# Performance work log

Measured on AMD Instinct MI355X. Metric: run time of the kernel, lower is better.

The kernel has to match this reference:

```python
import jax, jax.numpy as jnp
import numpy as np

IDIM = 1024
HIDDEN = 4096
N_EXPERT = 8
T = 2048


def setup_inputs() -> dict:
    key = jax.random.key(0)
    ks = jax.random.split(key, 6)
    s_in = 1.0 / np.sqrt(IDIM)
    s_h = 1.0 / np.sqrt(HIDDEN)
    return {
        "xs": jax.random.normal(ks[0], (T, IDIM), dtype=jnp.float32),
        "top_k": 2,
        # gate: Linear(idim -> n_expert, bias=False); torch weight (E, D)
        "Wg": jax.random.uniform(ks[1], (N_EXPERT, IDIM), jnp.float32, -s_in, s_in),
        # experts stacked: w_1 Linear(idim->hidden), w_2 Linear(hidden->idim)
        "W1": jax.random.uniform(ks[2], (N_EXPERT, IDIM, HIDDEN), jnp.float32, -s_in, s_in),
        "b1": jax.random.uniform(ks[3], (N_EXPERT, HIDDEN), jnp.float32, -s_in, s_in),
        "W2": jax.random.uniform(ks[4], (N_EXPERT, HIDDEN, IDIM), jnp.float32, -s_h, s_h),
        "b2": jax.random.uniform(ks[5], (N_EXPERT, IDIM), jnp.float32, -s_h, s_h),
    }


def reference(xs, top_k, Wg, W1, b1, W2, b2):
    # Router: (T, E)
    router = xs @ Wg.T
    logits, selected = jax.lax.top_k(router, top_k)          # (T, k)
    # softmax over the top-k slot axis in fp32, cast back (matches torch)
    weights = jax.nn.softmax(logits.astype(jnp.float32), axis=-1).astype(xs.dtype)
    # combine weight per token per expert: (T, E). Tokens not routed to an
    # expert get weight 0, zeroing that expert's contribution (same math as
    # the masked gather / scatter-add in the torch loop).
    onehot = jax.nn.one_hot(selected, N_EXPERT, dtype=xs.dtype)  # (T, k, E)
    comb = jnp.einsum("tk,tke->te", weights, onehot)
    # all-expert FFN (dropout_rate = 0 -> identity)
    h = jax.nn.relu(jnp.einsum("td,edh->teh", xs, W1) + b1[None, :, :])
    y = jnp.einsum("teh,ehd->ted", h, W2) + b2[None, :, :]
    return jnp.einsum("te,ted->td", comb, y)
```

## Files before the change

### kernel.cpp

```cpp
#include <hip/hip_runtime.h>
#include <hip/hip_bf16.h>
#include <stdint.h>

#define T_TOK 2048
#define IDIM  1024
#define HID   4096
#define NE    8
#define BM    128
#define BN    128
#define BK    64
#define RMAX  5120
#define MAXTILES 40

typedef __bf16 bf16;
typedef bf16  bf16x8 __attribute__((ext_vector_type(8)));
typedef float f32x4  __attribute__((ext_vector_type(4)));

#define WS_NTILES   128
#define WS_TILE_E   192
#define WS_TILE_R   448
#define WS_TOK_E    1024
#define WS_TOK_W    17408
#define WS_ROW_TOK  33792
#define WS_ROW_W    54272
#define WS_H        131072
#define WS_MIN_FAST ((size_t)WS_H + (size_t)RMAX * (HID / 32) * 2)

__global__ __launch_bounds__(256) void k_zero_out(float4* __restrict__ a) {
    a[blockIdx.x * 256 + threadIdx.x] = make_float4(0.f, 0.f, 0.f, 0.f);
}

__global__ __launch_bounds__(256) void k_router(const float* __restrict__ xs,
                                                const float* __restrict__ Wg,
                                                int* __restrict__ tok_e,
                                                float* __restrict__ tok_w) {
    __shared__ float sWg[NE * IDIM];
    for (int i = threadIdx.x; i < NE * IDIM; i += 256) sWg[i] = Wg[i];
    __syncthreads();
    int wave = threadIdx.x >> 6, lane = threadIdx.x & 63;
    int t = blockIdx.x * 4 + wave;
    if (t >= T_TOK) return;
    float p[NE];
#pragma unroll
    for (int e = 0; e < NE; e++) p[e] = 0.f;
    for (int j = 0; j < IDIM / 64; j++) {
        float x = xs[(size_t)t * IDIM + j * 64 + lane];
#pragma unroll
        for (int e = 0; e < NE; e++)
            p[e] += x * sWg[e * IDIM + j * 64 + lane];
    }
#pragma unroll
    for (int e = 0; e < NE; e++) {
        float v = p[e];
        for (int off = 32; off > 0; off >>= 1) v += __shfl_down(v, off);
        p[e] = v;
    }
    if (lane == 0) {
        int e0 = 0; float l0 = p[0];
        for (int e = 1; e < NE; e++) if (p[e] > l0) { l0 = p[e]; e0 = e; }
        int e1 = -1; float l1 = -1e30f;
        for (int e = 0; e < NE; e++) if (e != e0 && p[e] > l1) { l1 = p[e]; e1 = e; }
        if (e1 < 0) e1 = (e0 + 1) & 7;
        float z = __expf(l1 - l0);
        tok_e[2 * t]     = e0;  tok_e[2 * t + 1] = e1;
        tok_w[2 * t]     = 1.f / (1.f + z);
        tok_w[2 * t + 1] = z / (1.f + z);
    }
}

__global__ __launch_bounds__(256) void k_setup(int* __restrict__ w,
                                               float* __restrict__ wf) {
    __shared__ int cnt[NE];
    __shared__ int cur[NE];
    int tid = threadIdx.x;
    if (tid < NE) cnt[tid] = 0;
    for (int i = tid; i < RMAX; i += 256) w[WS_ROW_TOK / 4 + i] = -1;
    __syncthreads();
    for (int i = tid; i < 2 * T_TOK; i += 256)
        atomicAdd(&cnt[w[WS_TOK_E / 4 + i]], 1);
    __syncthreads();
    if (tid == 0) {
        int off = 0, nt = 0;
        for (int e = 0; e < NE; e++) {
            cur[e] = off;
            int nb = (cnt[e] + BM - 1) / BM;
            for (int b = 0; b < nb && nt < MAXTILES; b++) {
                w[WS_TILE_E / 4 + nt] = e;
                w[WS_TILE_R / 4 + nt] = off + b * BM;
                nt++;
            }
            off += nb * BM;
        }
        w[WS_NTILES / 4] = nt;
    }
    __syncthreads();
    for (int i = tid; i < 2 * T_TOK; i += 256) {
        int e   = w[WS_TOK_E / 4 + i];
        int pos = atomicAdd(&cur[e], 1);
        if (pos < RMAX) {
            w[WS_ROW_TOK / 4 + pos] = i >> 1;
            wf[WS_ROW_W / 4 + pos]  = wf[WS_TOK_W / 4 + i];
        }
    }
}

__device__ inline uint4 pack8(float4 a, float4 b) {
    union { bf16 h[8]; uint4 u; } pk;
    pk.h[0] = (bf16)a.x; pk.h[1] = (bf16)a.y; pk.h[2] = (bf16)a.z; pk.h[3] = (bf16)a.w;
    pk.h[4] = (bf16)b.x; pk.h[5] = (bf16)b.y; pk.h[6] = (bf16)b.z; pk.h[7] = (bf16)b.w;
    return pk.u;
}
__device__ inline uint32_t pack2(float a, float b) {
    union { bf16 h[2]; uint32_t u; } pk;
    pk.h[0] = (bf16)a; pk.h[1] = (bf16)b;
    return pk.u;
}

__global__ __launch_bounds__(256) void k_ffn1(const float* __restrict__ xs,
                                              const float* __restrict__ W1,
                                              const float* __restrict__ b1,
                                              const int* __restrict__ wsi,
                                              bf16* __restrict__ H,
                                              int h0, int CW) {
    int ntiles = wsi[WS_NTILES / 4];
    int tile = blockIdx.y;
    if (tile >= ntiles) return;
    int e    = wsi[WS_TILE_E / 4 + tile];
    int row0 = wsi[WS_TILE_R / 4 + tile];
    int n0l  = blockIdx.x * BN;
    int n0g  = h0 + n0l;

    const int*   row_tok = wsi + WS_ROW_TOK / 4;
    const float* Be      = W1 + (size_t)e * IDIM * HID;
    const float* bias_e  = b1 + (size_t)e * HID;

    __shared__ bf16 sA[BM * BK];
    __shared__ bf16 sB[BN * 72];

    int t    = threadIdx.x;
    int lane = t & 63, wv = t >> 6;
    int wx = wv & 1, wy = wv >> 1;
    int lm = lane & 15, q = lane >> 4;

    int rtk[4];
#pragma unroll
    for (int i = 0; i < 4; i++) rtk[i] = row_tok[row0 + (t >> 3) + i * 32];

    f32x4 acc[4][4];
#pragma unroll
    for (int i = 0; i < 4; i++)
#pragma unroll
        for (int j = 0; j < 4; j++) acc[i][j] = (f32x4){0.f, 0.f, 0.f, 0.f};

    for (int kc = 0; kc < IDIM / BK; kc++) {
        if (kc) __syncthreads();
#pragma unroll
        for (int i = 0; i < 4; i++) {
            int u = t + i * 256;
            int row = u >> 3, k8 = (u & 7) * 8;
            uint4 v;
            if (rtk[i] >= 0) {
                const float* g = xs + (size_t)rtk[i] * IDIM + kc * BK + k8;
                v = pack8(*(const float4*)g, *(const float4*)(g + 4));
            } else v = make_uint4(0u, 0u, 0u, 0u);
            *(uint4*)&sA[row * BK + k8] = v;
        }
#pragma unroll
        for (int i = 0; i < 2; i++) {
            int u = t + i * 256;
            int noct = u & 15, kp = u >> 4;
            int k = kp * 2;
            const float* g = Be + (size_t)(kc * BK + k) * HID + n0g + noct * 8;
            float4 r0a = *(const float4*)g;
            float4 r0b = *(const float4*)(g + 4);
            float4 r1a = *(const float4*)(g + HID);
            float4 r1b = *(const float4*)(g + HID + 4);
            float a0[8] = {r0a.x, r0a.y, r0a.z, r0a.w, r0b.x, r0b.y, r0b.z, r0b.w};
            float a1[8] = {r1a.x, r1a.y, r1a.z, r1a.w, r1b.x, r1b.y, r1b.z, r1b.w};
            int kswz = k ^ ((noct & 3) * 16);
            int hwb  = noct * 8 * 72 + kswz;
#pragma unroll
            for (int j = 0; j < 8; j++)
                *(uint32_t*)&sB[hwb + j * 72] = pack2(a0[j], a1[j]);
        }
        __syncthreads();
#pragma unroll
        for (int ks = 0; ks < 2; ks++) {
            bf16x8 aF[4], bF[4];
#pragma unroll
            for (int mt = 0; mt < 4; mt++)
                aF[mt] = *(bf16x8*)&sA[(wy * 64 + mt * 16 + lm) * BK + ks * 32 + q * 8];
#pragma unroll
            for (int nt = 0; nt < 4; nt++) {
                int n  = wx * 64 + nt * 16 + lm;
                int kk = (ks * 32 + q * 8) ^ (((n >> 3) & 3) * 16);
                bF[nt] = *(bf16x8*)&sB[n * 72 + kk];
            }
#pragma unroll
            for (int mt = 0; mt < 4; mt++)
#pragma unroll
                for (int nt = 0; nt < 4; nt++)
                    acc[mt][nt] = __builtin_amdgcn_mfma_f32_16x16x32_bf16(
                        aF[mt], bF[nt], acc[mt][nt], 0, 0, 0);
        }
    }

#pragma unroll
    for (int nt = 0; nt < 4; nt++) {
        int col_l = n0l + wx * 64 + nt * 16 + lm;
        float bv  = bias_e[h0 + col_l];
#pragma unroll
        for (int mt = 0; mt < 4; mt++) {
            int rloc = wy * 64 + mt * 16 + q * 4;
#pragma unroll
            for (int r = 0; r < 4; r++) {
                float v = fmaxf(acc[mt][nt][r] + bv, 0.f);
                H[(size_t)(row0 + rloc + r) * CW + col_l] = (bf16)v;
            }
        }
    }
}

__global__ __launch_bounds__(256) void k_ffn2(const bf16* __restrict__ H,
                                              const float* __restrict__ W2,
                                              const float* __restrict__ b2,
                                              const int* __restrict__ wsi,
                                              const float* __restrict__ wsf,
                                              float* __restrict__ out,
                                              int h0, int CW, int addb) {
    int ntiles = wsi[WS_NTILES / 4];
    int tile = blockIdx.y;
    if (tile >= ntiles) return;
    int e    = wsi[WS_TILE_E / 4 + tile];
    int row0 = wsi[WS_TILE_R / 4 + tile];
    int n0   = blockIdx.x * BN;
    int kw   = CW / gridDim.z;
    int kb   = blockIdx.z * kw;

    const int*   row_tok = wsi + WS_ROW_TOK / 4;
    const float* row_w   = wsf + WS_ROW_W / 4;
    const float* Be      = W2 + (size_t)e * HID * IDIM;
    const float* bias_e  = b2 + (size_t)e * IDIM;

    __shared__ bf16 sA[BM * BK];
    __shared__ bf16 sB[BN * 72];

    int t    = threadIdx.x;
    int lane = t & 63, wv = t >> 6;
    int wx = wv & 1, wy = wv >> 1;
    int lm = lane & 15, q = lane >> 4;

    f32x4 acc[4][4];
#pragma unroll
    for (int i = 0; i < 4; i++)
#pragma unroll
        for (int j = 0; j < 4; j++) acc[i][j] = (f32x4){0.f, 0.f, 0.f, 0.f};

    int kiters = kw / BK;
    for (int kc = 0; kc < kiters; kc++) {
        if (kc) __syncthreads();
#pragma unroll
        for (int i = 0; i < 4; i++) {
            int u = t + i * 256;
            int row = u >> 3, k8 = (u & 7) * 8;
            *(uint4*)&sA[row * BK + k8] =
                *(const uint4*)&H[(size_t)(row0 + row) * CW + kb + kc * BK + k8];
        }
#pragma unroll
        for (int i = 0; i < 2; i++) {
            int u = t + i * 256;
            int noct = u & 15, kp = u >> 4;
            int k = kp * 2;
            const float* g = Be + (size_t)(h0 + kb + kc * BK + k) * IDIM + n0 + noct * 8;
            float4 r0a = *(const float4*)g;
            float4 r0b = *(const float4*)(g + 4);
            float4 r1a = *(const float4*)(g + IDIM);
            float4 r1b = *(const float4*)(g + IDIM + 4);
            float a0[8] = {r0a.x, r0a.y, r0a.z, r0a.w, r0b.x, r0b.y, r0b.z, r0b.w};
            float a1[8] = {r1a.x, r1a.y, r1a.z, r1a.w, r1b.x, r1b.y, r1b.z, r1b.w};
            int kswz = k ^ ((noct & 3) * 16);
            int hwb  = noct * 8 * 72 + kswz;
#pragma unroll
            for (int j = 0; j < 8; j++)
                *(uint32_t*)&sB[hwb + j * 72] = pack2(a0[j], a1[j]);
        }
        __syncthreads();
#pragma unroll
        for (int ks = 0; ks < 2; ks++) {
            bf16x8 aF[4], bF[4];
#pragma unroll
            for (int mt = 0; mt < 4; mt++)
                aF[mt] = *(bf16x8*)&sA[(wy * 64 + mt * 16 + lm) * BK + ks * 32 + q * 8];
#pragma unroll
            for (int nt = 0; nt < 4; nt++) {
                int n  = wx * 64 + nt * 16 + lm;
                int kk = (ks * 32 + q * 8) ^ (((n >> 3) & 3) * 16);
                bF[nt] = *(bf16x8*)&sB[n * 72 + kk];
            }
#pragma unroll
            for (int mt = 0; mt < 4; mt++)
#pragma unroll
                for (int nt = 0; nt < 4; nt++)
                    acc[mt][nt] = __builtin_amdgcn_mfma_f32_16x16x32_bf16(
                        aF[mt], bF[nt], acc[mt][nt], 0, 0, 0);
        }
    }

    int   tokr[16];
    float wr[16];
#pragma unroll
    for (int mt = 0; mt < 4; mt++)
#pragma unroll
        for (int r = 0; r < 4; r++) {
            int rg = row0 + wy * 64 + mt * 16 + q * 4 + r;
            tokr[mt * 4 + r] = row_tok[rg];
            wr[mt * 4 + r]   = row_w[rg];
        }
    int dobias = addb && (blockIdx.z == 0);
#pragma unroll
    for (int nt = 0; nt < 4; nt++) {
        int col  = n0 + wx * 64 + nt * 16 + lm;
        float bv = dobias ? bias_e[col] : 0.f;
#pragma unroll
        for (int mt = 0; mt < 4; mt++)
#pragma unroll
            for (int r = 0; r < 4; r++) {
                int tok = tokr[mt * 4 + r];
                if (tok >= 0)
                    atomicAdd(&out[(size_t)tok * IDIM + col],
                              wr[mt * 4 + r] * (acc[mt][nt][r] + bv));
            }
    }
}

__global__ __launch_bounds__(256) void k_fallback(const float* __restrict__ xs,
                                                  const float* __restrict__ Wg,
                                                  const float* __restrict__ W1,
                                                  const float* __restrict__ b1,
                                                  const float* __restrict__ W2,
                                                  const float* __restrict__ b2,
                                                  float* __restrict__ out) {
    __shared__ float xbuf[IDIM];
    __shared__ float hbuf[256];
    __shared__ float slog[NE];
    __shared__ int   sel[2];
    __shared__ float selw[2];

    int t   = blockIdx.x;
    int tid = threadIdx.x;

    for (int i = tid; i < IDIM; i += 256)
        xbuf[i] = xs[(size_t)t * IDIM + i];
    __syncthreads();
    {
        int e = tid >> 5, l = tid & 31;
        float p = 0.f;
        for (int d = l; d < IDIM; d += 32)
            p += xbuf[d] * Wg[e * IDIM + d];
        for (int off = 16; off > 0; off >>= 1) p += __shfl_down(p, off, 32);
        if (l == 0) slog[e] = p;
    }
    __syncthreads();
    if (tid == 0) {
        int e0 = 0; float l0 = slog[0];
        for (int e = 1; e < NE; e++) if (slog[e] > l0) { l0 = slog[e]; e0 = e; }
        int e1 = -1; float l1 = -1e30f;
        for (int e = 0; e < NE; e++) if (e != e0 && slog[e] > l1) { l1 = slog[e]; e1 = e; }
        if (e1 < 0) e1 = (e0 + 1) & 7;
        float z = __expf(l1 - l0);
        sel[0] = e0; sel[1] = e1;
        selw[0] = 1.f / (1.f + z);
        selw[1] = z / (1.f + z);
    }
    __syncthreads();

    float ytot[4] = {0.f, 0.f, 0.f, 0.f};
#pragma unroll
    for (int s = 0; s < 2; s++) {
        int   e = sel[s];
        float w = selw[s];
        const float* W1e = W1 + (size_t)e * IDIM * HID;
        const float* W2e = W2 + (size_t)e * HID * IDIM;
        float ys[4] = {0.f, 0.f, 0.f, 0.f};
        for (int hb = 0; hb < HID / 256; hb++) {
            int h = hb * 256 + tid;
            float acc = b1[e * HID + h];
            for (int d = 0; d < IDIM; d++)
                acc += xbuf[d] * W1e[(size_t)d * HID + h];
            __syncthreads();
            hbuf[tid] = fmaxf(acc, 0.f);
            __syncthreads();
            for (int hh = 0; hh < 256; hh++) {
                float hv = hbuf[hh];
                const float* wrow = W2e + (size_t)(hb * 256 + hh) * IDIM;
#pragma unroll
                for (int cc = 0; cc < 4; cc++)
                    ys[cc] += hv * wrow[cc * 256 + tid];
            }
        }
#pragma unroll
        for (int cc = 0; cc < 4; cc++)
            ytot[cc] += w * (ys[cc] + b2[e * IDIM + cc * 256 + tid]);
    }
#pragma unroll
    for (int cc = 0; cc < 4; cc++)
        out[(size_t)t * IDIM + cc * 256 + tid] = ytot[cc];
}

extern "C" void kernel_launch(void* const* d_in, const int* in_sizes, int n_in,
                              void* d_out, int out_size, void* d_ws, size_t ws_size,
                              hipStream_t stream) {
    int o = (n_in >= 7 && in_sizes[1] == 1) ? 1 : 0;
    const float* xs = (const float*)d_in[0];
    const float* Wg = (const float*)d_in[1 + o];
    const float* W1 = (const float*)d_in[2 + o];
    const float* b1 = (const float*)d_in[3 + o];
    const float* W2 = (const float*)d_in[4 + o];
    const float* b2 = (const float*)d_in[5 + o];
    float* out = (float*)d_out;

    if (ws_size < WS_MIN_FAST || d_ws == nullptr) {
        k_fallback<<<T_TOK, 256, 0, stream>>>(xs, Wg, W1, b1, W2, b2, out);
        return;
    }

    char*  ws  = (char*)d_ws;
    int*   wsi = (int*)d_ws;
    float* wsf = (float*)d_ws;
    bf16*  H   = (bf16*)(ws + WS_H);

    int HC = 1;
    while (HC < 32 &&
           (size_t)WS_H + (size_t)RMAX * (HID / HC) * 2 > ws_size)
        HC <<= 1;
    int CW = HID / HC;
    int SK = 4;
    while (CW / SK < BK) SK >>= 1;

    k_zero_out<<<T_TOK, 256, 0, stream>>>((float4*)out);
    k_router<<<T_TOK / 4, 256, 0, stream>>>(xs, Wg, wsi + WS_TOK_E / 4,
                                            wsf + WS_TOK_W / 4);
    k_setup<<<1, 256, 0, stream>>>(wsi, wsf);

    for (int c = 0; c < HC; c++) {
        k_ffn1<<<dim3(CW / BN, MAXTILES), 256, 0, stream>>>(
            xs, W1, b1, wsi, H, c * CW, CW);
        k_ffn2<<<dim3(IDIM / BN, MAXTILES, SK), 256, 0, stream>>>(
            H, W2, b2, wsi, wsf, out, c * CW, CW, c == 0 ? 1 : 0);
    }
}
```

Measured before the change: 515.7 us.

## Pre-convert weights and gathered activations to swizzled bf16, load via global_load_lds

Adds a gather kernel that packs routed token rows into a bf16 buffer and a conversion kernel that transposes and converts W1/W2 into k-contiguous, XOR-swizzled bf16 tiles in the workspace. The FFN GEMMs then stream tiles straight into LDS with global_load_lds, with no in-loop fp32-to-bf16 conversion or scattered activation reads. FFN2 drops split-K in favour of narrower 64-column tiles, which cuts the atomic traffic to the output. The cost is extra passes that read all weights and write a bf16 copy on every call, plus a larger workspace requirement.

```diff
diff --git a/kernel.cpp b/kernel.cpp
--- a/kernel.cpp
+++ b/kernel.cpp
@@ -1,5 +1,4 @@
 #include <hip/hip_runtime.h>
-#include <hip/hip_bf16.h>
 #include <stdint.h>
 
 #define T_TOK 2048
@@ -8,6 +7,7 @@
 #define NE    8
 #define BM    128
 #define BN    128
+#define BN2   64
 #define BK    64
 #define RMAX  5120
 #define MAXTILES 40
@@ -23,8 +23,7 @@
 #define WS_TOK_W    17408
 #define WS_ROW_TOK  33792
 #define WS_ROW_W    54272
-#define WS_H        131072
-#define WS_MIN_FAST ((size_t)WS_H + (size_t)RMAX * (HID / 32) * 2)
+#define XG_OFF      131072
 
 __global__ __launch_bounds__(256) void k_zero_out(float4* __restrict__ a) {
     a[blockIdx.x * 256 + threadIdx.x] = make_float4(0.f, 0.f, 0.f, 0.f);
@@ -116,35 +115,86 @@
     return pk.u;
 }
 
-__global__ __launch_bounds__(256) void k_ffn1(const float* __restrict__ xs,
-                                              const float* __restrict__ W1,
-                                              const float* __restrict__ b1,
-                                              const int* __restrict__ wsi,
-                                              bf16* __restrict__ H,
-                                              int h0, int CW) {
-    int ntiles = wsi[WS_NTILES / 4];
+__device__ __forceinline__ void g2l16(const bf16* g, bf16* l) {
+    __builtin_amdgcn_global_load_lds(
+        (const __attribute__((address_space(1))) void*)g,
+        (__attribute__((address_space(3))) void*)l, 16, 0, 0);
+}
+
+__global__ __launch_bounds__(256) void k_gather(const float* __restrict__ xs,
+                                                const int* __restrict__ wsi,
+                                                bf16* __restrict__ Xg) {
+    int wv = threadIdx.x >> 6, lane = threadIdx.x & 63;
+    int r = blockIdx.x * 4 + wv;
+    int tok = wsi[WS_ROW_TOK / 4 + r];
+#pragma unroll
+    for (int i = 0; i < 2; i++) {
+        int c = i * 64 + lane;
+        uint4 v;
+        if (tok >= 0) {
+            const float* g = xs + (size_t)tok * IDIM + c * 8;
+            v = pack8(*(const float4*)g, *(const float4*)(g + 4));
+        } else v = make_uint4(0u, 0u, 0u, 0u);
+        int cs = (c & ~7) | ((c & 7) ^ (r & 7));
+        *(uint4*)&Xg[(size_t)r * IDIM + cs * 8] = v;
+    }
+}
+
+__global__ __launch_bounds__(256) void k_cvt(const float* __restrict__ src,
+                                             bf16* __restrict__ dst,
+                                             int ld_src, int k0, int n0, int KL,
+                                             size_t s_estride, size_t d_estride) {
+    __shared__ bf16 sT[64 * 66];
+    int e = blockIdx.y;
+    const float* S = src + (size_t)e * s_estride;
+    bf16* D = dst + (size_t)e * d_estride;
+    int ntk = KL >> 6;
+    int tk = blockIdx.x % ntk, tn = blockIdx.x / ntk;
+    int t = threadIdx.x;
+#pragma unroll
+    for (int i = 0; i < 4; i++) {
+        int idx = t + i * 256;
+        int k = idx >> 4, n4 = (idx & 15) * 4;
+        float4 v = *(const float4*)&S[(size_t)(k0 + tk * 64 + k) * ld_src +
+                                      n0 + tn * 64 + n4];
+        *(uint32_t*)&sT[k * 66 + n4]     = pack2(v.x, v.y);
+        *(uint32_t*)&sT[k * 66 + n4 + 2] = pack2(v.z, v.w);
+    }
+    __syncthreads();
+#pragma unroll
+    for (int j = 0; j < 2; j++) {
+        int idx = t + j * 256;
+        int n = idx >> 3, kq = idx & 7;
+        union { bf16 h[8]; uint4 u; } pk;
+#pragma unroll
+        for (int jj = 0; jj < 8; jj++) pk.h[jj] = sT[(kq * 8 + jj) * 66 + n];
+        int ng = tn * 64 + n;
+        int ch = kq ^ (ng & 7);
+        *(uint4*)&D[(size_t)ng * KL + tk * 64 + ch * 8] = pk.u;
+    }
+}
+
+__global__ __launch_bounds__(256) void k_ffn1n(const bf16* __restrict__ Xg,
+                                               const bf16* __restrict__ W1t,
+                                               const float* __restrict__ b1,
+                                               const int* __restrict__ wsi,
+                                               bf16* __restrict__ H,
+                                               int h0, int CW) {
     int tile = blockIdx.y;
-    if (tile >= ntiles) return;
+    if (tile >= wsi[WS_NTILES / 4]) return;
     int e    = wsi[WS_TILE_E / 4 + tile];
     int row0 = wsi[WS_TILE_R / 4 + tile];
-    int n0l  = blockIdx.x * BN;
-    int n0g  = h0 + n0l;
-
-    const int*   row_tok = wsi + WS_ROW_TOK / 4;
-    const float* Be      = W1 + (size_t)e * IDIM * HID;
-    const float* bias_e  = b1 + (size_t)e * HID;
+    int n0   = blockIdx.x * BN;
+
+    const bf16* Abase = Xg + (size_t)row0 * IDIM;
+    const bf16* Bbase = W1t + ((size_t)e * CW + n0) * IDIM;
 
     __shared__ bf16 sA[BM * BK];
-    __shared__ bf16 sB[BN * 72];
-
-    int t    = threadIdx.x;
-    int lane = t & 63, wv = t >> 6;
-    int wx = wv & 1, wy = wv >> 1;
+    __shared__ bf16 sB[BN * BK];
+
+    int t = threadIdx.x, lane = t & 63;
+    int wv = t >> 6, wx = wv & 1, wy = wv >> 1;
     int lm = lane & 15, q = lane >> 4;
-
-    int rtk[4];
-#pragma unroll
-    for (int i = 0; i < 4; i++) rtk[i] = row_tok[row0 + (t >> 3) + i * 32];
 
     f32x4 acc[4][4];
 #pragma unroll
@@ -156,45 +206,29 @@
         if (kc) __syncthreads();
 #pragma unroll
         for (int i = 0; i < 4; i++) {
-            int u = t + i * 256;
-            int row = u >> 3, k8 = (u & 7) * 8;
-            uint4 v;
-            if (rtk[i] >= 0) {
-                const float* g = xs + (size_t)rtk[i] * IDIM + kc * BK + k8;
-                v = pack8(*(const float4*)g, *(const float4*)(g + 4));
-            } else v = make_uint4(0u, 0u, 0u, 0u);
-            *(uint4*)&sA[row * BK + k8] = v;
-        }
-#pragma unroll
-        for (int i = 0; i < 2; i++) {
-            int u = t + i * 256;
-            int noct = u & 15, kp = u >> 4;
-            int k = kp * 2;
-            const float* g = Be + (size_t)(kc * BK + k) * HID + n0g + noct * 8;
-            float4 r0a = *(const float4*)g;
-            float4 r0b = *(const float4*)(g + 4);
-            float4 r1a = *(const float4*)(g + HID);
-            float4 r1b = *(const float4*)(g + HID + 4);
-            float a0[8] = {r0a.x, r0a.y, r0a.z, r0a.w, r0b.x, r0b.y, r0b.z, r0b.w};
-            float a1[8] = {r1a.x, r1a.y, r1a.z, r1a.w, r1b.x, r1b.y, r1b.z, r1b.w};
-            int kswz = k ^ ((noct & 3) * 16);
-            int hwb  = noct * 8 * 72 + kswz;
-#pragma unroll
-            for (int j = 0; j < 8; j++)
-                *(uint32_t*)&sB[hwb + j * 72] = pack2(a0[j], a1[j]);
+            int s = t + i * 256;
+            g2l16(Abase + (size_t)(s >> 3) * IDIM + kc * BK + (s & 7) * 8,
+                  &sA[s * 8]);
+        }
+#pragma unroll
+        for (int i = 0; i < 4; i++) {
+            int s = t + i * 256;
+            g2l16(Bbase + (size_t)(s >> 3) * IDIM + kc * BK + (s & 7) * 8,
+                  &sB[s * 8]);
         }
         __syncthreads();
 #pragma unroll
         for (int ks = 0; ks < 2; ks++) {
             bf16x8 aF[4], bF[4];
 #pragma unroll
-            for (int mt = 0; mt < 4; mt++)
-                aF[mt] = *(bf16x8*)&sA[(wy * 64 + mt * 16 + lm) * BK + ks * 32 + q * 8];
+            for (int mt = 0; mt < 4; mt++) {
+                int r = wy * 64 + mt * 16 + lm;
+                aF[mt] = *(const bf16x8*)&sA[r * BK + (((ks * 4 + q) ^ (r & 7)) * 8)];
+            }
 #pragma unroll
             for (int nt = 0; nt < 4; nt++) {
-                int n  = wx * 64 + nt * 16 + lm;
-                int kk = (ks * 32 + q * 8) ^ (((n >> 3) & 3) * 16);
-                bF[nt] = *(bf16x8*)&sB[n * 72 + kk];
+                int r = wx * 64 + nt * 16 + lm;
+                bF[nt] = *(const bf16x8*)&sB[r * BK + (((ks * 4 + q) ^ (r & 7)) * 8)];
             }
 #pragma unroll
             for (int mt = 0; mt < 4; mt++)
@@ -204,103 +238,86 @@
                         aF[mt], bF[nt], acc[mt][nt], 0, 0, 0);
         }
     }
-
 #pragma unroll
     for (int nt = 0; nt < 4; nt++) {
-        int col_l = n0l + wx * 64 + nt * 16 + lm;
-        float bv  = bias_e[h0 + col_l];
+        int col = n0 + wx * 64 + nt * 16 + lm;
+        float bv = b1[(size_t)e * HID + h0 + col];
 #pragma unroll
         for (int mt = 0; mt < 4; mt++) {
-            int rloc = wy * 64 + mt * 16 + q * 4;
 #pragma unroll
             for (int r = 0; r < 4; r++) {
+                int rg = row0 + wy * 64 + mt * 16 + q * 4 + r;
                 float v = fmaxf(acc[mt][nt][r] + bv, 0.f);
-                H[(size_t)(row0 + rloc + r) * CW + col_l] = (bf16)v;
-            }
-        }
-    }
-}
-
-__global__ __launch_bounds__(256) void k_ffn2(const bf16* __restrict__ H,
-                                              const float* __restrict__ W2,
-                                              const float* __restrict__ b2,
-                                              const int* __restrict__ wsi,
-                                              const float* __restrict__ wsf,
-                                              float* __restrict__ out,
-                                              int h0, int CW, int addb) {
-    int ntiles = wsi[WS_NTILES / 4];
+                int sc = (col & ~63) | ((col & 63) ^ ((rg & 7) << 3));
+                H[(size_t)rg * CW + sc] = (bf16)v;
+            }
+        }
+    }
+}
+
+__global__ __launch_bounds__(256) void k_ffn2n(const bf16* __restrict__ H,
+                                               const bf16* __restrict__ W2t,
+                                               const float* __restrict__ b2,
+                                               const int* __restrict__ wsi,
+                                               const float* __restrict__ wsf,
+                                               float* __restrict__ out,
+                                               int CW, int addb) {
     int tile = blockIdx.y;
-    if (tile >= ntiles) return;
+    if (tile >= wsi[WS_NTILES / 4]) return;
     int e    = wsi[WS_TILE_E / 4 + tile];
     int row0 = wsi[WS_TILE_R / 4 + tile];
-    int n0   = blockIdx.x * BN;
-    int kw   = CW / gridDim.z;
-    int kb   = blockIdx.z * kw;
+    int n0   = blockIdx.x * BN2;
 
     const int*   row_tok = wsi + WS_ROW_TOK / 4;
     const float* row_w   = wsf + WS_ROW_W / 4;
-    const float* Be      = W2 + (size_t)e * HID * IDIM;
-    const float* bias_e  = b2 + (size_t)e * IDIM;
+    const bf16* Abase = H + (size_t)row0 * CW;
+    const bf16* Bbase = W2t + ((size_t)e * IDIM + n0) * CW;
 
     __shared__ bf16 sA[BM * BK];
-    __shared__ bf16 sB[BN * 72];
-
-    int t    = threadIdx.x;
-    int lane = t & 63, wv = t >> 6;
-    int wx = wv & 1, wy = wv >> 1;
+    __shared__ bf16 sB[BN2 * BK];
+
+    int t = threadIdx.x, lane = t & 63;
+    int wv = t >> 6, wx = wv & 1, wy = wv >> 1;
     int lm = lane & 15, q = lane >> 4;
 
-    f32x4 acc[4][4];
+    f32x4 acc[4][2];
 #pragma unroll
     for (int i = 0; i < 4; i++)
 #pragma unroll
-        for (int j = 0; j < 4; j++) acc[i][j] = (f32x4){0.f, 0.f, 0.f, 0.f};
-
-    int kiters = kw / BK;
-    for (int kc = 0; kc < kiters; kc++) {
+        for (int j = 0; j < 2; j++) acc[i][j] = (f32x4){0.f, 0.f, 0.f, 0.f};
+
+    for (int kc = 0; kc < CW / BK; kc++) {
         if (kc) __syncthreads();
 #pragma unroll
         for (int i = 0; i < 4; i++) {
-            int u = t + i * 256;
-            int row = u >> 3, k8 = (u & 7) * 8;
-            *(uint4*)&sA[row * BK + k8] =
-                *(const uint4*)&H[(size_t)(row0 + row) * CW + kb + kc * BK + k8];
+            int s = t + i * 256;
+            g2l16(Abase + (size_t)(s >> 3) * CW + kc * BK + (s & 7) * 8,
+                  &sA[s * 8]);
         }
 #pragma unroll
         for (int i = 0; i < 2; i++) {
-            int u = t + i * 256;
-            int noct = u & 15, kp = u >> 4;
-            int k = kp * 2;
-            const float* g = Be + (size_t)(h0 + kb + kc * BK + k) * IDIM + n0 + noct * 8;
-            float4 r0a = *(const float4*)g;
-            float4 r0b = *(const float4*)(g + 4);
-            float4 r1a = *(const float4*)(g + IDIM);
-            float4 r1b = *(const float4*)(g + IDIM + 4);
-            float a0[8] = {r0a.x, r0a.y, r0a.z, r0a.w, r0b.x, r0b.y, r0b.z, r0b.w};
-            float a1[8] = {r1a.x, r1a.y, r1a.z, r1a.w, r1b.x, r1b.y, r1b.z, r1b.w};
-            int kswz = k ^ ((noct & 3) * 16);
-            int hwb  = noct * 8 * 72 + kswz;
-#pragma unroll
-            for (int j = 0; j < 8; j++)
-                *(uint32_t*)&sB[hwb + j * 72] = pack2(a0[j], a1[j]);
+            int s = t + i * 256;
+            g2l16(Bbase + (size_t)(s >> 3) * CW + kc * BK + (s & 7) * 8,
+                  &sB[s * 8]);
         }
         __syncthreads();
 #pragma unroll
         for (int ks = 0; ks < 2; ks++) {
-            bf16x8 aF[4], bF[4];
+            bf16x8 aF[4], bF[2];
+#pragma unroll
+            for (int mt = 0; mt < 4; mt++) {
+                int r = wy * 64 + mt * 16 + lm;
+                aF[mt] = *(const bf16x8*)&sA[r * BK + (((ks * 4 + q) ^ (r & 7)) * 8)];
+            }
+#pragma unroll
+            for (int nt = 0; nt < 2; nt++) {
+                int r = wx * 32 + nt * 16 + lm;
+                bF[nt] = *(const bf16x8*)&sB[r * BK + (((ks * 4 + q) ^ (r & 7)) * 8)];
+            }
 #pragma unroll
             for (int mt = 0; mt < 4; mt++)
-                aF[mt] = *(bf16x8*)&sA[(wy * 64 + mt * 16 + lm) * BK + ks * 32 + q * 8];
-#pragma unroll
-            for (int nt = 0; nt < 4; nt++) {
-                int n  = wx * 64 + nt * 16 + lm;
-                int kk = (ks * 32 + q * 8) ^ (((n >> 3) & 3) * 16);
-                bF[nt] = *(bf16x8*)&sB[n * 72 + kk];
-            }
-#pragma unroll
-            for (int mt = 0; mt < 4; mt++)
-#pragma unroll
-                for (int nt = 0; nt < 4; nt++)
+#pragma unroll
+                for (int nt = 0; nt < 2; nt++)
                     acc[mt][nt] = __builtin_amdgcn_mfma_f32_16x16x32_bf16(
                         aF[mt], bF[nt], acc[mt][nt], 0, 0, 0);
         }
@@ -316,11 +333,10 @@
             tokr[mt * 4 + r] = row_tok[rg];
             wr[mt * 4 + r]   = row_w[rg];
         }
-    int dobias = addb && (blockIdx.z == 0);
-#pragma unroll
-    for (int nt = 0; nt < 4; nt++) {
-        int col  = n0 + wx * 64 + nt * 16 + lm;
-        float bv = dobias ? bias_e[col] : 0.f;
+#pragma unroll
+    for (int nt = 0; nt < 2; nt++) {
+        int col  = n0 + wx * 32 + nt * 16 + lm;
+        float bv = addb ? b2[(size_t)e * IDIM + col] : 0.f;
 #pragma unroll
         for (int mt = 0; mt < 4; mt++)
 #pragma unroll
@@ -419,7 +435,16 @@
     const float* b2 = (const float*)d_in[5 + o];
     float* out = (float*)d_out;
 
-    if (ws_size < WS_MIN_FAST || d_ws == nullptr) {
+    size_t xg_sz = (size_t)RMAX * IDIM * 2;
+    int CW = 0;
+    if (d_ws) {
+        for (int c = HID; c >= 512; c >>= 1) {
+            size_t need = (size_t)XG_OFF + xg_sz + (size_t)RMAX * c * 2 +
+                          (size_t)NE * c * IDIM * 2;
+            if (ws_size >= need) { CW = c; break; }
+        }
+    }
+    if (!CW) {
         k_fallback<<<T_TOK, 256, 0, stream>>>(xs, Wg, W1, b1, W2, b2, out);
         return;
     }
@@ -427,25 +452,27 @@
     char*  ws  = (char*)d_ws;
     int*   wsi = (int*)d_ws;
     float* wsf = (float*)d_ws;
-    bf16*  H   = (bf16*)(ws + WS_H);
-
-    int HC = 1;
-    while (HC < 32 &&
-           (size_t)WS_H + (size_t)RMAX * (HID / HC) * 2 > ws_size)
-        HC <<= 1;
-    int CW = HID / HC;
-    int SK = 4;
-    while (CW / SK < BK) SK >>= 1;
+    bf16*  Xg  = (bf16*)(ws + XG_OFF);
+    bf16*  Hb  = (bf16*)(ws + XG_OFF + xg_sz);
+    bf16*  Wt  = (bf16*)(ws + XG_OFF + xg_sz + (size_t)RMAX * CW * 2);
 
     k_zero_out<<<T_TOK, 256, 0, stream>>>((float4*)out);
     k_router<<<T_TOK / 4, 256, 0, stream>>>(xs, Wg, wsi + WS_TOK_E / 4,
                                             wsf + WS_TOK_W / 4);
     k_setup<<<1, 256, 0, stream>>>(wsi, wsf);
-
+    k_gather<<<RMAX / 4, 256, 0, stream>>>(xs, wsi, Xg);
+
+    int HC = HID / CW;
     for (int c = 0; c < HC; c++) {
-        k_ffn1<<<dim3(CW / BN, MAXTILES), 256, 0, stream>>>(
-            xs, W1, b1, wsi, H, c * CW, CW);
-        k_ffn2<<<dim3(IDIM / BN, MAXTILES, SK), 256, 0, stream>>>(
-            H, W2, b2, wsi, wsf, out, c * CW, CW, c == 0 ? 1 : 0);
-    }
-}
+        k_cvt<<<dim3((IDIM / 64) * (CW / 64), NE), 256, 0, stream>>>(
+            W1, Wt, HID, 0, c * CW, IDIM,
+            (size_t)IDIM * HID, (size_t)CW * IDIM);
+        k_ffn1n<<<dim3(CW / BN, MAXTILES), 256, 0, stream>>>(
+            Xg, Wt, b1, wsi, Hb, c * CW, CW);
+        k_cvt<<<dim3((CW / 64) * (IDIM / 64), NE), 256, 0, stream>>>(
+            W2, Wt, IDIM, c * CW, 0, CW,
+            (size_t)HID * IDIM, (size_t)IDIM * CW);
+        k_ffn2n<<<dim3(IDIM / BN2, MAXTILES), 256, 0, stream>>>(
+            Hb, Wt, b2, wsi, wsf, out, CW, c == 0 ? 1 : 0);
+    }
+}
```

Measured after the change: 441.7 us. 14.3% less time.
